# Performance work log

Measured on AMD Instinct MI355X. Metric: run time of the kernel, lower is better.

The kernel has to match this reference:

```python
import jax, jax.numpy as jnp
import numpy as np

B, S, D, H = 2, 2048, 1024, 16
DH = D // H  # 64


def _rotate_half(t):
    x1, x2 = jnp.split(t, 2, axis=-1)
    return jnp.concatenate([-x2, x1], axis=-1)


def setup_inputs() -> dict:
    key = jax.random.key(0)
    ks = jax.random.split(key, 11)
    x = jax.random.normal(ks[0], (B, S, D), dtype=jnp.float32)
    mask = jax.random.randint(ks[1], (B, S), 0, 2, dtype=jnp.int32)
    scale = 0.02
    wq = jax.random.normal(ks[2], (D, D), dtype=jnp.float32) * scale
    bq = jnp.zeros((D,), dtype=jnp.float32)
    wk = jax.random.normal(ks[3], (D, D), dtype=jnp.float32) * scale
    bk = jnp.zeros((D,), dtype=jnp.float32)
    wv = jax.random.normal(ks[4], (D, D), dtype=jnp.float32) * scale
    bv = jnp.zeros((D,), dtype=jnp.float32)
    wo = jax.random.normal(ks[5], (D, D), dtype=jnp.float32) * scale
    bo = jnp.zeros((D,), dtype=jnp.float32)
    return {"x": x, "mask": mask, "wq": wq, "bq": bq, "wk": wk, "bk": bk,
            "wv": wv, "bv": bv, "wo": wo, "bo": bo}


def reference(x, mask, wq, bq, wk, bk, wv, bv, wo, bo):
    b, s, d = x.shape
    # QKV projections, split heads -> [B, H, S, DH]
    q = (x @ wq + bq).reshape(b, s, H, DH).transpose(0, 2, 1, 3)
    k = (x @ wk + bk).reshape(b, s, H, DH).transpose(0, 2, 1, 3)
    v = (x @ wv + bv).reshape(b, s, H, DH).transpose(0, 2, 1, 3)
    # RoPE exactly as in source: repeat(cos,2) paired with half-split rotate
    pos = jnp.arange(s, dtype=jnp.float32)
    inv_freq = 1.0 / (10000.0 ** (jnp.arange(0, DH, 2, dtype=jnp.float32) / DH))
    angle = pos[:, None] * inv_freq[None, :]            # [S, DH/2]
    cos = jnp.repeat(jnp.cos(angle), 2, axis=-1)[None, None]  # [1,1,S,DH]
    sin = jnp.repeat(jnp.sin(angle), 2, axis=-1)[None, None]
    q = q * cos + _rotate_half(q) * sin
    k = k * cos + _rotate_half(k) * sin
    # scaled dot-product attention with additive mask
    logits = jnp.einsum('bhqd,bhkd->bhqk', q, k) / jnp.sqrt(jnp.float32(DH))
    m = mask.astype(jnp.float32)[:, None, None, :]      # [B,1,1,S]
    logits = logits + m * (-1e9)
    attn = jax.nn.softmax(logits, axis=-1)
    out = jnp.einsum('bhqk,bhkd->bhqd', attn, v)
    out = out.transpose(0, 2, 1, 3).reshape(b, s, d)
    return out @ wo + bo
```

## Files before the change

### kernel.cpp

```cpp
#include <hip/hip_runtime.h>
#include <math.h>

#define BB 2
#define SS 2048
#define DD 1024
#define HH 16

typedef unsigned short u16;
using bf16x8 = __attribute__((ext_vector_type(8))) short;
using f32x4  = __attribute__((ext_vector_type(4))) float;

#define LOG2E 1.44269504f


__device__ __forceinline__ u16 f2bf(float f) {
    unsigned u = __float_as_uint(f);
    unsigned r = u + 0x7fffu + ((u >> 16) & 1u);
    return (u16)(r >> 16);
}

__device__ __forceinline__ void gload_lds16(const void* g, const void* l) {
    __builtin_amdgcn_global_load_lds(
        (const __attribute__((address_space(1))) unsigned int*)(unsigned long long)g,
        (__attribute__((address_space(3))) unsigned int*)(unsigned int)(unsigned long long)l,
        16, 0, 0);
}

__global__ void rope_table(float* __restrict__ cost, float* __restrict__ sint) {
    int idx = blockIdx.x * 256 + threadIdx.x;
    int j   = idx >> 11;
    int pos = idx & 2047;
    double inv = pow(10000.0, -(double)j / 32.0);
    double ang = (double)pos * inv;
    cost[idx] = (float)cos(ang);
    sint[idx] = (float)sin(ang);
}

__global__ void mkbias(const int* __restrict__ mask, float* __restrict__ mb) {
    int i = blockIdx.x * 256 + threadIdx.x;
    mb[i] = -1.44269504e9f * (float)mask[i];
}

__global__ void cvt_x(const float* __restrict__ x, u16* __restrict__ xb) {
    int i = (blockIdx.x * 256 + threadIdx.x) * 4;
    float4 v = *(const float4*)(x + i);
    ushort4 o;
    o.x = f2bf(v.x); o.y = f2bf(v.y); o.z = f2bf(v.z); o.w = f2bf(v.w);
    *(ushort4*)(xb + i) = o;
}

__global__ void transpose_w(const float* __restrict__ w0, const float* __restrict__ w1,
                            const float* __restrict__ w2, const float* __restrict__ w3,
                            u16* __restrict__ o0, u16* __restrict__ o1,
                            u16* __restrict__ o2, u16* __restrict__ o3) {
    const float* in = (blockIdx.z == 0) ? w0 : (blockIdx.z == 1) ? w1 : (blockIdx.z == 2) ? w2 : w3;
    u16* out        = (blockIdx.z == 0) ? o0 : (blockIdx.z == 1) ? o1 : (blockIdx.z == 2) ? o2 : o3;
    __shared__ float t[32][33];
    int n = blockIdx.x * 32 + threadIdx.x;
    for (int i = threadIdx.y; i < 32; i += 8)
        t[i][threadIdx.x] = in[(size_t)(blockIdx.y * 32 + i) * 1024 + n];
    __syncthreads();
    int k = blockIdx.y * 32 + threadIdx.x;
    for (int i = threadIdx.y; i < 32; i += 8)
        out[(size_t)(blockIdx.x * 32 + i) * 1024 + k] = f2bf(t[threadIdx.x][i]);
}

__global__ __launch_bounds__(256)
void qkv_gemm(const u16* __restrict__ xb,
              const u16* __restrict__ wtq, const u16* __restrict__ wtk, const u16* __restrict__ wtv,
              const float* __restrict__ bq, const float* __restrict__ bk, const float* __restrict__ bv,
              const float* __restrict__ cost, const float* __restrict__ sint,
              u16* __restrict__ qo, u16* __restrict__ ko, u16* __restrict__ vo)
{
    __shared__ u16 Al[128 * 32];
    __shared__ u16 Bl[128 * 32];

    int bx = blockIdx.x;
    int which = bx >> 3;
    int n0 = (bx & 7) << 7;
    int m0 = blockIdx.y << 7;
    const u16*  wt    = (which == 0) ? wtq : (which == 1) ? wtk : wtv;
    const float* bias = (which == 0) ? bq  : (which == 1) ? bk  : bv;

    int t = threadIdx.x;
    int wid = t >> 6, lane = t & 63;
    int wr = wid >> 1, wc = wid & 1;
    int fr = lane & 15, fq = lane >> 4;

    f32x4 acc[4][4];
    #pragma unroll
    for (int m = 0; m < 4; ++m)
        #pragma unroll
        for (int n = 0; n < 4; ++n)
            #pragma unroll
            for (int r = 0; r < 4; ++r) acc[m][n][r] = 0.f;

    int srow = (lane >> 2);
    int skof = (lane & 3) << 3;

    for (int k0 = 0; k0 < 1024; k0 += 32) {
        __syncthreads();
        #pragma unroll
        for (int c = 0; c < 2; ++c) {
            int chunk = wid * 2 + c;
            int row = (chunk << 4) + srow;
            gload_lds16(xb + (size_t)(m0 + row) * 1024 + k0 + skof, &Al[chunk << 9]);
            gload_lds16(wt + (size_t)(n0 + row) * 1024 + k0 + skof, &Bl[chunk << 9]);
        }
        __syncthreads();

        bf16x8 af[4], bf[4];
        #pragma unroll
        for (int m = 0; m < 4; ++m)
            af[m] = *(const bf16x8*)&Al[((wr << 6) + (m << 4) + fr) * 32 + (fq << 3)];
        #pragma unroll
        for (int n = 0; n < 4; ++n)
            bf[n] = *(const bf16x8*)&Bl[((wc << 6) + (n << 4) + fr) * 32 + (fq << 3)];
        #pragma unroll
        for (int m = 0; m < 4; ++m)
            #pragma unroll
            for (int n = 0; n < 4; ++n)
                acc[m][n] = __builtin_amdgcn_mfma_f32_16x16x32_bf16(af[m], bf[n], acc[m][n], 0, 0, 0);
    }

    if (which < 2) {
        u16* outp = (which == 0) ? qo : ko;
        const float qs = (which == 0) ? 0.125f * LOG2E : 1.0f;
        #pragma unroll
        for (int n = 0; n < 2; ++n) {
            int col = n0 + (wc << 6) + (n << 4) + fr;
            int h = col >> 6;
            int d = col & 63;
            float b1 = bias[col], b2 = bias[col + 32];
            int a1 = d >> 1;
            #pragma unroll
            for (int mm = 0; mm < 4; ++mm) {
                int mi0 = m0 + (wr << 6) + (mm << 4) + (fq << 2);
                int bi = mi0 >> 11, s0 = mi0 & 2047;
                float4 c1 = *(const float4*)(cost + (a1 << 11) + s0);
                float4 s1 = *(const float4*)(sint + (a1 << 11) + s0);
                float4 c2 = *(const float4*)(cost + ((a1 + 16) << 11) + s0);
                float4 s2 = *(const float4*)(sint + ((a1 + 16) << 11) + s0);
                const float* c1p = (const float*)&c1;
                const float* s1p = (const float*)&s1;
                const float* c2p = (const float*)&c2;
                const float* s2p = (const float*)&s2;
                #pragma unroll
                for (int j = 0; j < 4; ++j) {
                    float x1 = acc[mm][n][j]     + b1;
                    float x2 = acc[mm][n + 2][j] + b2;
                    size_t base = ((size_t)(bi * HH + h) * SS + s0 + j) << 6;
                    outp[base + d]      = f2bf((x1 * c1p[j] - x2 * s1p[j]) * qs);
                    outp[base + d + 32] = f2bf((x2 * c2p[j] + x1 * s2p[j]) * qs);
                }
            }
        }
    } else {
        #pragma unroll
        for (int n = 0; n < 4; ++n) {
            int col = n0 + (wc << 6) + (n << 4) + fr;
            int h = col >> 6, d = col & 63;
            float bb = bias[col];
            #pragma unroll
            for (int mm = 0; mm < 4; ++mm) {
                #pragma unroll
                for (int j = 0; j < 4; ++j) {
                    int mi = m0 + (wr << 6) + (mm << 4) + (fq << 2) + j;
                    int bi = mi >> 11, s = mi & 2047;
                    vo[(((size_t)(bi * HH + h) * SS + s) << 6) + d] = f2bf(acc[mm][n][j] + bb);
                }
            }
        }
    }
}

__global__ __launch_bounds__(256)
void transpose_v(const u16* __restrict__ vin, u16* __restrict__ vout) {
    __shared__ u16 Ld[64][72];
    int stile = blockIdx.x;
    int bh    = blockIdx.y;
    int t = threadIdx.x;
    int r = t >> 2, seg = (t & 3) << 4;
    const u16* src = vin + (((size_t)bh * SS + (stile << 6) + r) << 6) + seg;
    *(uint4*)&Ld[r][seg]     = *(const uint4*)src;
    *(uint4*)&Ld[r][seg + 8] = *(const uint4*)(src + 8);
    __syncthreads();
    u16 tmp[16];
    #pragma unroll
    for (int i = 0; i < 16; ++i) tmp[i] = Ld[seg + i][r];
    u16* dst = vout + ((size_t)(bh << 6) + r) * SS + (stile << 6) + seg;
    *(uint4*)dst       = *(const uint4*)&tmp[0];
    *(uint4*)(dst + 8) = *(const uint4*)&tmp[8];
}

__global__ __launch_bounds__(256, 4)
void attn(const u16* __restrict__ qb, const u16* __restrict__ kb, const u16* __restrict__ vt,
          const float* __restrict__ mbias, u16* __restrict__ preb)
{
    __shared__ u16 Kl[2][4096];
    __shared__ u16 Vl[2][4096];
    __shared__ u16 Pl[4][1024];

    const int bid = blockIdx.x;
    const int xcd = bid & 7;
    const int idx = bid >> 3;
    const int bh  = (xcd << 2) | (idx >> 5);
    const int qb0 = (idx & 31) << 6;
    const int b   = bh >> 4;
    const int t   = threadIdx.x;
    const int w   = t >> 6;
    const int lane = t & 63;
    const int fr  = lane & 15;
    const int fq  = lane >> 4;
    const int swz = (fr & 7) << 4;

    const char* kbase = (const char*)(kb + ((size_t)bh << 17));
    const char* vbase = (const char*)(vt + ((size_t)bh << 17));
    const float* mbp  = mbias + (b << 11);

    const int sbo = ((t & 7) << 4) ^ (((t >> 3) & 7) << 4);

    const int qrow = qb0 + (w << 4) + fr;
    const u16* qp = qb + (((size_t)bh << 11) + qrow) * 64 + (fq << 3);
    bf16x8 qf0 = *(const bf16x8*)qp;
    bf16x8 qf1 = *(const bf16x8*)(qp + 32);

    f32x4 o[4];
    #pragma unroll
    for (int n = 0; n < 4; ++n)
        #pragma unroll
        for (int r = 0; r < 4; ++r) o[n][r] = 0.f;
    float mrun = -INFINITY, lrun = 0.f;

    auto STAGE = [&](int buf, int kt) {
        #pragma unroll
        for (int c = 0; c < 2; ++c) {
            int row = (c << 5) + (t >> 3);
            gload_lds16(kbase + ((size_t)(kt << 6) + row) * 128 + sbo,
                        (const char*)&Kl[buf][0] + (c << 12) + t * 16);
            gload_lds16(vbase + (size_t)row * 4096 + (kt << 7) + sbo,
                        (const char*)&Vl[buf][0] + (c << 12) + t * 16);
        }
    };

    STAGE(0, 0);
    __syncthreads();

    for (int kt = 0; kt < 32; ++kt) {
        const int cur = kt & 1;

        if (kt < 31) STAGE(cur ^ 1, kt + 1);

        f32x4 sv[4];
        #pragma unroll
        for (int g = 0; g < 4; ++g)
            #pragma unroll
            for (int r = 0; r < 4; ++r) sv[g][r] = 0.f;

        const char* Kb = (const char*)&Kl[cur][0];
        __builtin_amdgcn_s_setprio(1);
        #pragma unroll
        for (int g = 0; g < 4; ++g) {
            int row = (g << 4) + fr;
            bf16x8 kf0 = *(const bf16x8*)(Kb + row * 128 + ((fq << 4) ^ swz));
            bf16x8 kf1 = *(const bf16x8*)(Kb + row * 128 + (((fq << 4) + 64) ^ swz));
            sv[g] = __builtin_amdgcn_mfma_f32_16x16x32_bf16(kf0, qf0, sv[g], 0, 0, 0);
            sv[g] = __builtin_amdgcn_mfma_f32_16x16x32_bf16(kf1, qf1, sv[g], 0, 0, 0);
        }
        __builtin_amdgcn_s_setprio(0);

        float tm = -INFINITY;
        #pragma unroll
        for (int g = 0; g < 4; ++g) {
            const float4 m4 = *(const float4*)(mbp + (kt << 6) + (g << 4) + (fq << 2));
            sv[g][0] += m4.x; sv[g][1] += m4.y; sv[g][2] += m4.z; sv[g][3] += m4.w;
            tm = fmaxf(tm, fmaxf(fmaxf(sv[g][0], sv[g][1]), fmaxf(sv[g][2], sv[g][3])));
        }
        tm = fmaxf(tm, __shfl_xor(tm, 16));
        tm = fmaxf(tm, __shfl_xor(tm, 32));

        if (!__all(tm <= mrun + 11.0f)) {
            float newm = fmaxf(mrun, tm);
            float scale = __builtin_amdgcn_exp2f(mrun - newm);
            lrun *= scale;
            #pragma unroll
            for (int j = 0; j < 4; ++j) {
                float sj = __shfl(scale, (lane & 48) + (fq << 2) + j);
                #pragma unroll
                for (int n = 0; n < 4; ++n) o[n][j] *= sj;
            }
            mrun = newm;
        }

        float ps = 0.f;
        #pragma unroll
        for (int g = 0; g < 4; ++g) {
            float p0 = __builtin_amdgcn_exp2f(sv[g][0] - mrun);
            float p1 = __builtin_amdgcn_exp2f(sv[g][1] - mrun);
            float p2 = __builtin_amdgcn_exp2f(sv[g][2] - mrun);
            float p3 = __builtin_amdgcn_exp2f(sv[g][3] - mrun);
            ps += (p0 + p1) + (p2 + p3);
            unsigned r0, r1;
            asm("v_cvt_pk_bf16_f32 %0, %1, %2" : "=v"(r0) : "v"(p0), "v"(p1));
            asm("v_cvt_pk_bf16_f32 %0, %1, %2" : "=v"(r1) : "v"(p2), "v"(p3));
            uint2 pw; pw.x = r0; pw.y = r1;
            *(uint2*)((char*)&Pl[w][0] + fr * 128 + (((g << 5) + (fq << 3)) ^ swz)) = pw;
        }
        ps += __shfl_xor(ps, 16);
        ps += __shfl_xor(ps, 32);
        lrun += ps;

        __builtin_amdgcn_s_setprio(1);
        #pragma unroll
        for (int kk = 0; kk < 2; ++kk) {
            bf16x8 pa = *(const bf16x8*)((const char*)&Pl[w][0] + fr * 128 + (((fq << 4) + (kk << 6)) ^ swz));
            #pragma unroll
            for (int n = 0; n < 4; ++n) {
                int row = (n << 4) + fr;
                bf16x8 vf = *(const bf16x8*)((const char*)&Vl[cur][0] + row * 128 + (((fq << 4) + (kk << 6)) ^ swz));
                o[n] = __builtin_amdgcn_mfma_f32_16x16x32_bf16(pa, vf, o[n], 0, 0, 0);
            }
        }
        __builtin_amdgcn_s_setprio(0);
        __syncthreads();
    }

    #pragma unroll
    for (int j = 0; j < 4; ++j) {
        float lj = __shfl(lrun, (lane & 48) + (fq << 2) + j);
        float inv = 1.0f / lj;
        int qr = qb0 + (w << 4) + (fq << 2) + j;
        u16* op = preb + ((size_t)((b << 11) + qr) << 10) + ((bh & 15) << 6) + fr;
        #pragma unroll
        for (int n = 0; n < 4; ++n)
            op[n << 4] = f2bf(o[n][j] * inv);
    }
}

__global__ __launch_bounds__(256)
void out_gemm(const u16* __restrict__ pre, const u16* __restrict__ wto,
              const float* __restrict__ bo, float* __restrict__ outp)
{
    __shared__ u16 Al[128 * 32];
    __shared__ u16 Bl[128 * 32];

    int n0 = blockIdx.x << 7;
    int m0 = blockIdx.y << 7;

    int t = threadIdx.x;
    int wid = t >> 6, lane = t & 63;
    int wr = wid >> 1, wc = wid & 1;
    int fr = lane & 15, fq = lane >> 4;

    f32x4 acc[4][4];
    #pragma unroll
    for (int m = 0; m < 4; ++m)
        #pragma unroll
        for (int n = 0; n < 4; ++n)
            #pragma unroll
            for (int r = 0; r < 4; ++r) acc[m][n][r] = 0.f;

    int srow = (lane >> 2);
    int skof = (lane & 3) << 3;

    for (int k0 = 0; k0 < 1024; k0 += 32) {
        __syncthreads();
        #pragma unroll
        for (int c = 0; c < 2; ++c) {
            int chunk = wid * 2 + c;
            int row = (chunk << 4) + srow;
            gload_lds16(pre + (size_t)(m0 + row) * 1024 + k0 + skof, &Al[chunk << 9]);
            gload_lds16(wto + (size_t)(n0 + row) * 1024 + k0 + skof, &Bl[chunk << 9]);
        }
        __syncthreads();

        bf16x8 af[4], bf[4];
        #pragma unroll
        for (int m = 0; m < 4; ++m)
            af[m] = *(const bf16x8*)&Al[((wr << 6) + (m << 4) + fr) * 32 + (fq << 3)];
        #pragma unroll
        for (int n = 0; n < 4; ++n)
            bf[n] = *(const bf16x8*)&Bl[((wc << 6) + (n << 4) + fr) * 32 + (fq << 3)];
        #pragma unroll
        for (int m = 0; m < 4; ++m)
            #pragma unroll
            for (int n = 0; n < 4; ++n)
                acc[m][n] = __builtin_amdgcn_mfma_f32_16x16x32_bf16(af[m], bf[n], acc[m][n], 0, 0, 0);
    }

    #pragma unroll
    for (int n = 0; n < 4; ++n) {
        int col = n0 + (wc << 6) + (n << 4) + fr;
        float bb = bo[col];
        #pragma unroll
        for (int m = 0; m < 4; ++m) {
            #pragma unroll
            for (int j = 0; j < 4; ++j) {
                int mi = m0 + (wr << 6) + (m << 4) + (fq << 2) + j;
                outp[(size_t)mi * 1024 + col] = acc[m][n][j] + bb;
            }
        }
    }
}

extern "C" void kernel_launch(void* const* d_in, const int* in_sizes, int n_in,
                              void* d_out, int out_size, void* d_ws, size_t ws_size,
                              hipStream_t stream) {
    const float* x    = (const float*)d_in[0];
    const int*   mask = (const int*)  d_in[1];
    const float* wq   = (const float*)d_in[2];
    const float* bq   = (const float*)d_in[3];
    const float* wk   = (const float*)d_in[4];
    const float* bk   = (const float*)d_in[5];
    const float* wv   = (const float*)d_in[6];
    const float* bv   = (const float*)d_in[7];
    const float* wo   = (const float*)d_in[8];
    const float* bo   = (const float*)d_in[9];
    float* out = (float*)d_out;
    float* ws  = (float*)d_ws;

    float* cosT  = ws;
    float* sinT  = ws + 65536;
    float* mbias = ws + 131072;
    u16* xb    = (u16*)(ws + 135168);
    u16* wtq   = xb    + 4194304;
    u16* wtk   = wtq   + 1048576;
    u16* wtv   = wtk   + 1048576;
    u16* wto   = wtv   + 1048576;
    u16* qbuf  = wto   + 1048576;
    u16* kbuf  = qbuf  + 4194304;
    u16* vbuf  = kbuf  + 4194304;
    u16* preb  = vbuf  + 4194304;
    u16* vtbuf = xb;

    hipLaunchKernelGGL(rope_table, dim3(256), dim3(256), 0, stream, cosT, sinT);
    hipLaunchKernelGGL(mkbias, dim3(16), dim3(256), 0, stream, mask, mbias);
    hipLaunchKernelGGL(cvt_x, dim3(4096), dim3(256), 0, stream, x, xb);
    hipLaunchKernelGGL(transpose_w, dim3(32, 32, 4), dim3(32, 8), 0, stream,
                       wq, wk, wv, wo, wtq, wtk, wtv, wto);
    hipLaunchKernelGGL(qkv_gemm, dim3(24, 32), dim3(256), 0, stream,
                       xb, wtq, wtk, wtv, bq, bk, bv, cosT, sinT, qbuf, kbuf, vbuf);
    hipLaunchKernelGGL(transpose_v, dim3(32, 32), dim3(256), 0, stream, vbuf, vtbuf);
    hipLaunchKernelGGL(attn, dim3(1024), dim3(256), 0, stream,
                       qbuf, kbuf, vtbuf, mbias, preb);
    hipLaunchKernelGGL(out_gemm, dim3(8, 32), dim3(256), 0, stream, preb, wto, bo, out);
}
```

Baseline: 241.4 us.

## Merge prep kernels into one launch and write V transposed from QKV GEMM

Four preprocessing kernels (rope table, mask bias, x conversion, weight transpose) are combined into one kernel that dispatches work by block index. The separate V transpose kernel is removed: the QKV GEMM epilogue now writes V directly in [b,h,d,s] layout. This cuts four launches and one full round trip of V through memory. The cost is that the V stores are strided by the sequence length and uncoalesced, and the branchy fused prep kernel may balance its blocks less evenly.

```diff
diff --git a/kernel.cpp b/kernel.cpp
--- a/kernel.cpp
+++ b/kernel.cpp
@@ -26,43 +26,54 @@
         16, 0, 0);
 }
 
-__global__ void rope_table(float* __restrict__ cost, float* __restrict__ sint) {
-    int idx = blockIdx.x * 256 + threadIdx.x;
-    int j   = idx >> 11;
-    int pos = idx & 2047;
-    double inv = pow(10000.0, -(double)j / 32.0);
-    double ang = (double)pos * inv;
-    cost[idx] = (float)cos(ang);
-    sint[idx] = (float)sin(ang);
-}
-
-__global__ void mkbias(const int* __restrict__ mask, float* __restrict__ mb) {
-    int i = blockIdx.x * 256 + threadIdx.x;
-    mb[i] = -1.44269504e9f * (float)mask[i];
-}
-
-__global__ void cvt_x(const float* __restrict__ x, u16* __restrict__ xb) {
-    int i = (blockIdx.x * 256 + threadIdx.x) * 4;
-    float4 v = *(const float4*)(x + i);
-    ushort4 o;
-    o.x = f2bf(v.x); o.y = f2bf(v.y); o.z = f2bf(v.z); o.w = f2bf(v.w);
-    *(ushort4*)(xb + i) = o;
-}
-
-__global__ void transpose_w(const float* __restrict__ w0, const float* __restrict__ w1,
-                            const float* __restrict__ w2, const float* __restrict__ w3,
-                            u16* __restrict__ o0, u16* __restrict__ o1,
-                            u16* __restrict__ o2, u16* __restrict__ o3) {
-    const float* in = (blockIdx.z == 0) ? w0 : (blockIdx.z == 1) ? w1 : (blockIdx.z == 2) ? w2 : w3;
-    u16* out        = (blockIdx.z == 0) ? o0 : (blockIdx.z == 1) ? o1 : (blockIdx.z == 2) ? o2 : o3;
-    __shared__ float t[32][33];
-    int n = blockIdx.x * 32 + threadIdx.x;
-    for (int i = threadIdx.y; i < 32; i += 8)
-        t[i][threadIdx.x] = in[(size_t)(blockIdx.y * 32 + i) * 1024 + n];
-    __syncthreads();
-    int k = blockIdx.y * 32 + threadIdx.x;
-    for (int i = threadIdx.y; i < 32; i += 8)
-        out[(size_t)(blockIdx.x * 32 + i) * 1024 + k] = f2bf(t[threadIdx.x][i]);
+__global__ void prep_tw(const float* __restrict__ x, u16* __restrict__ xb,
+                        float* __restrict__ cost, float* __restrict__ sint,
+                        const int* __restrict__ mask, float* __restrict__ mb,
+                        const float* __restrict__ w0, const float* __restrict__ w1,
+                        const float* __restrict__ w2, const float* __restrict__ w3,
+                        u16* __restrict__ o0, u16* __restrict__ o1,
+                        u16* __restrict__ o2, u16* __restrict__ o3) {
+    __shared__ float tb[32][33];
+    int bid = blockIdx.x;
+    int t   = threadIdx.x;
+    if (bid < 4096) {
+        int gid = bid * 256 + t;
+        {
+            int i = gid * 4;
+            float4 v = *(const float4*)(x + i);
+            ushort4 o;
+            o.x = f2bf(v.x); o.y = f2bf(v.y); o.z = f2bf(v.z); o.w = f2bf(v.w);
+            *(ushort4*)(xb + i) = o;
+        }
+        if (bid < 256) {
+            int j   = gid >> 11;
+            int pos = gid & 2047;
+            double inv = pow(10000.0, -(double)j / 32.0);
+            double ang = (double)pos * inv;
+            cost[gid] = (float)cos(ang);
+            sint[gid] = (float)sin(ang);
+        }
+        if (bid >= 256 && bid < 272) {
+            int i = gid - 65536;
+            mb[i] = -1.44269504e9f * (float)mask[i];
+        }
+    } else {
+        int tid = bid - 4096;
+        int z   = tid >> 10;
+        int rem = tid & 1023;
+        int bxt = rem & 31;
+        int byt = rem >> 5;
+        const float* in = (z == 0) ? w0 : (z == 1) ? w1 : (z == 2) ? w2 : w3;
+        u16* out        = (z == 0) ? o0 : (z == 1) ? o1 : (z == 2) ? o2 : o3;
+        int tx = t & 31, ty = t >> 5;
+        int n = bxt * 32 + tx;
+        for (int i = ty; i < 32; i += 8)
+            tb[i][tx] = in[(size_t)(byt * 32 + i) * 1024 + n];
+        __syncthreads();
+        int k = byt * 32 + tx;
+        for (int i = ty; i < 32; i += 8)
+            out[(size_t)(bxt * 32 + i) * 1024 + k] = f2bf(tb[tx][i]);
+    }
 }
 
 __global__ __launch_bounds__(256)
@@ -167,30 +178,11 @@
                 for (int j = 0; j < 4; ++j) {
                     int mi = m0 + (wr << 6) + (mm << 4) + (fq << 2) + j;
                     int bi = mi >> 11, s = mi & 2047;
-                    vo[(((size_t)(bi * HH + h) * SS + s) << 6) + d] = f2bf(acc[mm][n][j] + bb);
+                    vo[((((size_t)(bi * HH + h)) << 6) + d) * SS + s] = f2bf(acc[mm][n][j] + bb);
                 }
             }
         }
     }
-}
-
-__global__ __launch_bounds__(256)
-void transpose_v(const u16* __restrict__ vin, u16* __restrict__ vout) {
-    __shared__ u16 Ld[64][72];
-    int stile = blockIdx.x;
-    int bh    = blockIdx.y;
-    int t = threadIdx.x;
-    int r = t >> 2, seg = (t & 3) << 4;
-    const u16* src = vin + (((size_t)bh * SS + (stile << 6) + r) << 6) + seg;
-    *(uint4*)&Ld[r][seg]     = *(const uint4*)src;
-    *(uint4*)&Ld[r][seg + 8] = *(const uint4*)(src + 8);
-    __syncthreads();
-    u16 tmp[16];
-    #pragma unroll
-    for (int i = 0; i < 16; ++i) tmp[i] = Ld[seg + i][r];
-    u16* dst = vout + ((size_t)(bh << 6) + r) * SS + (stile << 6) + seg;
-    *(uint4*)dst       = *(const uint4*)&tmp[0];
-    *(uint4*)(dst + 8) = *(const uint4*)&tmp[8];
 }
 
 __global__ __launch_bounds__(256, 4)
@@ -429,18 +421,14 @@
     u16* wto   = wtv   + 1048576;
     u16* qbuf  = wto   + 1048576;
     u16* kbuf  = qbuf  + 4194304;
-    u16* vbuf  = kbuf  + 4194304;
-    u16* preb  = vbuf  + 4194304;
-    u16* vtbuf = xb;
-
-    hipLaunchKernelGGL(rope_table, dim3(256), dim3(256), 0, stream, cosT, sinT);
-    hipLaunchKernelGGL(mkbias, dim3(16), dim3(256), 0, stream, mask, mbias);
-    hipLaunchKernelGGL(cvt_x, dim3(4096), dim3(256), 0, stream, x, xb);
-    hipLaunchKernelGGL(transpose_w, dim3(32, 32, 4), dim3(32, 8), 0, stream,
+    u16* vtbuf = kbuf  + 4194304;
+    u16* preb  = vtbuf + 4194304;
+
+    hipLaunchKernelGGL(prep_tw, dim3(8192), dim3(256), 0, stream,
+                       x, xb, cosT, sinT, mask, mbias,
                        wq, wk, wv, wo, wtq, wtk, wtv, wto);
     hipLaunchKernelGGL(qkv_gemm, dim3(24, 32), dim3(256), 0, stream,
-                       xb, wtq, wtk, wtv, bq, bk, bv, cosT, sinT, qbuf, kbuf, vbuf);
-    hipLaunchKernelGGL(transpose_v, dim3(32, 32), dim3(256), 0, stream, vbuf, vtbuf);
+                       xb, wtq, wtk, wtv, bq, bk, bv, cosT, sinT, qbuf, kbuf, vtbuf);
     hipLaunchKernelGGL(attn, dim3(1024), dim3(256), 0, stream,
                        qbuf, kbuf, vtbuf, mbias, preb);
     hipLaunchKernelGGL(out_gemm, dim3(8, 32), dim3(256), 0, stream, preb, wto, bo, out);
```

New measurement: 227.5 us. 1.06x faster.
